# Kernel optimization log

Measured on AMD Instinct MI355X. Metric: run time of the kernel, lower is better.

Reference implementation:

```python
import jax, jax.numpy as jnp
import numpy as np

B, T, IN, H, OUT = 512, 1000, 39, 64, 48


def setup_inputs() -> dict:
    key = jax.random.key(0)
    ks = jax.random.split(key, 7)
    s = 1.0 / np.sqrt(H)
    return {
        "x": jax.random.normal(ks[0], (B, T, IN), dtype=jnp.float32),
        "W_ih": jax.random.uniform(ks[1], (4 * H, IN), minval=-s, maxval=s, dtype=jnp.float32),
        "W_hh": jax.random.uniform(ks[2], (4 * H, H), minval=-s, maxval=s, dtype=jnp.float32),
        "b_ih": jax.random.uniform(ks[3], (4 * H,), minval=-s, maxval=s, dtype=jnp.float32),
        "b_hh": jax.random.uniform(ks[4], (4 * H,), minval=-s, maxval=s, dtype=jnp.float32),
        "W_out": jax.random.uniform(ks[5], (OUT, H), minval=-s, maxval=s, dtype=jnp.float32),
        "b_out": jax.random.uniform(ks[6], (OUT,), minval=-s, maxval=s, dtype=jnp.float32),
    }


def reference(x, W_ih, W_hh, b_ih, b_hh, W_out, b_out):
    # Single-layer batch-first LSTM (zero init state) + per-step Linear + sigmoid.
    b = b_ih + b_hh  # [4H]
    # Precompute input projections for all timesteps at once: [T, B, 4H]
    xg = jnp.einsum('bti,gi->tbg', x, W_ih) + b

    def step(carry, xg_t):
        h, c = carry
        gates = xg_t + h @ W_hh.T  # [B, 4H], gate order i, f, g, o
        i, f, g, o = jnp.split(gates, 4, axis=-1)
        c = jax.nn.sigmoid(f) * c + jax.nn.sigmoid(i) * jnp.tanh(g)
        h = jax.nn.sigmoid(o) * jnp.tanh(c)
        y = jax.nn.sigmoid(h @ W_out.T + b_out)  # [B, OUT]
        return (h, c), y

    h0 = jnp.zeros((x.shape[0], W_hh.shape[1]), dtype=x.dtype)
    (_, _), ys = jax.lax.scan(step, (h0, h0), xg)  # ys: [T, B, OUT]
    return jnp.swapaxes(ys, 0, 1)  # [B, T, OUT]
```

## Files before the change

kernel.cpp:

```cpp
#include <hip/hip_runtime.h>


#define BB 512
#define TT 1000
#define INF 39
#define HH 64
#define OUTF 48
#define G4 (4 * HH)

#define Q10(M) M(0) M(1) M(2) M(3) M(4) M(5) M(6) M(7) M(8) M(9)
#define Q16(M) M(0) M(1) M(2) M(3) M(4) M(5) M(6) M(7) \
               M(8) M(9) M(10) M(11) M(12) M(13) M(14) M(15)

__global__ __launch_bounds__(256, 2) void lstm_fused_kernel(
    const float* __restrict__ x,
    const float* __restrict__ W_ih,
    const float* __restrict__ W_hh,
    const float* __restrict__ b_ih,
    const float* __restrict__ b_hh,
    const float* __restrict__ W_out,
    const float* __restrict__ b_out,
    float* __restrict__ out)
{
    const int b = blockIdx.x;
    const int tid = threadIdx.x;

    __shared__ float xs[40];
    __shared__ float hs[HH];
    __shared__ float act[G4];

    const float* wih_ptr = W_ih + tid * INF;
#define LOAD_IH4(q) float4 wiq##q; \
    wiq##q.x = wih_ptr[4*(q)]; \
    wiq##q.y = (4*(q)+1 < INF) ? wih_ptr[4*(q)+1] : 0.f; \
    wiq##q.z = (4*(q)+2 < INF) ? wih_ptr[4*(q)+2] : 0.f; \
    wiq##q.w = (4*(q)+3 < INF) ? wih_ptr[4*(q)+3] : 0.f;
    Q10(LOAD_IH4)

    const float4* wh4p = (const float4*)(W_hh + tid * HH);
#define LOAD_HH4(i) const float4 wh##i = wh4p[i];
    Q16(LOAD_HH4)

    const float bias = b_ih[tid] + b_hh[tid];

    const int o = tid >> 2;
    const int p = tid & 3;
    float4 wo0, wo1, wo2, wo3;
    float bo = 0.f;
    if (tid < 4 * OUTF) {
        const float4* wop = (const float4*)(W_out + o * HH + p * 16);
        wo0 = wop[0]; wo1 = wop[1]; wo2 = wop[2]; wo3 = wop[3];
        bo = b_out[o];
    } else {
        wo0 = wo1 = wo2 = wo3 = make_float4(0.f, 0.f, 0.f, 0.f);
    }

    float c = 0.f;
    const size_t x_base = (size_t)b * TT * INF;
    const size_t out_base = (size_t)b * TT * OUTF;

    if (tid < HH) hs[tid] = 0.f;
    if (tid < INF) xs[tid] = x[x_base + tid];
    if (tid == 39) xs[39] = 0.f;
    float xreg = (tid < INF) ? x[x_base + INF + tid] : 0.f;

    const int gate_type = tid >> 6;
    __syncthreads();

    const float4* xs4 = (const float4*)xs;
    const float4* hs4 = (const float4*)hs;

    for (int t = 0; t < TT; ++t) {
        float a0 = bias, a1 = 0.f, a2 = 0.f, a3 = 0.f;
#define FMA_IH4(q) { const float4 xv = xs4[q]; \
        a0 += xv.x * wiq##q.x; a1 += xv.y * wiq##q.y; \
        a2 += xv.z * wiq##q.z; a3 += xv.w * wiq##q.w; }
        Q10(FMA_IH4)
#define FMA_HH4(i) { const float4 hv = hs4[i]; \
        a0 += hv.x * wh##i.x; a1 += hv.y * wh##i.y; \
        a2 += hv.z * wh##i.z; a3 += hv.w * wh##i.w; }
        Q16(FMA_HH4)
        const float acc = (a0 + a1) + (a2 + a3);

        float a;
        if (gate_type == 2) {
            a = 2.f / (1.f + __expf(-2.f * acc)) - 1.f;
        } else {
            a = 1.f / (1.f + __expf(-acc));
        }
        act[tid] = a;
        __syncthreads();

        if (tid < INF) {
            xs[tid] = xreg;
            if (t + 2 < TT) xreg = x[x_base + (size_t)(t + 2) * INF + tid];
        }
        if (tid < HH) {
            const float ig = act[tid];
            const float fg = act[HH + tid];
            const float gg = act[2 * HH + tid];
            const float og = act[3 * HH + tid];
            c = fg * c + ig * gg;
            const float th = 2.f / (1.f + __expf(-2.f * c)) - 1.f;
            hs[tid] = og * th;
        }
        __syncthreads();

        if (tid < 4 * OUTF) {
            const float4 h0 = hs4[p * 4 + 0];
            const float4 h1 = hs4[p * 4 + 1];
            const float4 h2 = hs4[p * 4 + 2];
            const float4 h3 = hs4[p * 4 + 3];
            float s0 = h0.x * wo0.x + h0.y * wo0.y + h0.z * wo0.z + h0.w * wo0.w;
            float s1 = h1.x * wo1.x + h1.y * wo1.y + h1.z * wo1.z + h1.w * wo1.w;
            float s2 = h2.x * wo2.x + h2.y * wo2.y + h2.z * wo2.z + h2.w * wo2.w;
            float s3 = h3.x * wo3.x + h3.y * wo3.y + h3.z * wo3.z + h3.w * wo3.w;
            float s = (s0 + s1) + (s2 + s3);
            s += __shfl_xor(s, 1, 64);
            s += __shfl_xor(s, 2, 64);
            if (p == 0) {
                const float y = 1.f / (1.f + __expf(-(s + bo)));
                __builtin_nontemporal_store(y, &out[out_base + (size_t)t * OUTF + o]);
            }
        }
    }
}

extern "C" void kernel_launch(void* const* d_in, const int* in_sizes, int n_in,
                              void* d_out, int out_size, void* d_ws, size_t ws_size,
                              hipStream_t stream) {
    const float* x     = (const float*)d_in[0];
    const float* W_ih  = (const float*)d_in[1];
    const float* W_hh  = (const float*)d_in[2];
    const float* b_ih  = (const float*)d_in[3];
    const float* b_hh  = (const float*)d_in[4];
    const float* W_out = (const float*)d_in[5];
    const float* b_out = (const float*)d_in[6];
    float* out = (float*)d_out;

    lstm_fused_kernel<<<dim3(BB), dim3(G4), 0, stream>>>(
        x, W_ih, W_hh, b_ih, b_hh, W_out, b_out, out);
}
```

Measured before the change: 1.076 ms.

## Rewrite LSTM kernel: two sequences per block, K-split waves, one barrier per step

Each block now handles two batch rows. The 256 threads are split into 4 waves, and each wave owns a K-slice of the recurrent and input contractions for all four gates of hidden unit j. h and x values are broadcast across lanes with readlane instead of being read from shared memory. Partial sums are reduced through double-buffered shared arrays, so each timestep needs a single barrier, and the output projection is delayed by one step so it overlaps with the next step's work. A prepack kernel rearranges the weights into a gate-interleaved layout in the workspace. The trade-offs are half as many blocks, W_ih reloaded from global memory every step, and an occupancy hint of 1.

New measurement: 1.311 ms. +21.8%, slower.

```diff
diff --git a/kernel.cpp b/kernel.cpp
--- a/kernel.cpp
+++ b/kernel.cpp
@@ -6,122 +6,221 @@
 #define INF 39
 #define HH 64
 #define OUTF 48
-#define G4 (4 * HH)
-
-#define Q10(M) M(0) M(1) M(2) M(3) M(4) M(5) M(6) M(7) M(8) M(9)
-#define Q16(M) M(0) M(1) M(2) M(3) M(4) M(5) M(6) M(7) \
-               M(8) M(9) M(10) M(11) M(12) M(13) M(14) M(15)
-
-__global__ __launch_bounds__(256, 2) void lstm_fused_kernel(
-    const float* __restrict__ x,
-    const float* __restrict__ W_ih,
-    const float* __restrict__ W_hh,
-    const float* __restrict__ b_ih,
-    const float* __restrict__ b_hh,
-    const float* __restrict__ W_out,
-    const float* __restrict__ b_out,
-    float* __restrict__ out)
+
+typedef float v2f __attribute__((ext_vector_type(2)));
+
+__device__ __forceinline__ float sigf(float v)  { return 1.f / (1.f + __expf(-v)); }
+__device__ __forceinline__ float tanhx(float v) { return 2.f / (1.f + __expf(-2.f * v)) - 1.f; }
+
+#define RLF(VB, L) __int_as_float(__builtin_amdgcn_readlane((VB), (L)))
+
+__global__ void pack_weights(const float* __restrict__ W_ih,
+                             const float* __restrict__ W_hh,
+                             float4* __restrict__ ws) {
+    const int idx = blockIdx.x * 256 + threadIdx.x;
+    if (idx < 40 * 64) {
+        const int i = idx >> 6, j = idx & 63;
+        float4 v = make_float4(0.f, 0.f, 0.f, 0.f);
+        if (i < INF) {
+            v.x = W_ih[(0 * HH + j) * INF + i];
+            v.y = W_ih[(1 * HH + j) * INF + i];
+            v.z = W_ih[(2 * HH + j) * INF + i];
+            v.w = W_ih[(3 * HH + j) * INF + i];
+        }
+        ws[idx] = v;
+    } else if (idx < 40 * 64 + HH * 64) {
+        const int t = idx - 40 * 64;
+        const int k = t >> 6, j = t & 63;
+        ws[idx] = make_float4(W_hh[(0 * HH + j) * HH + k], W_hh[(1 * HH + j) * HH + k],
+                              W_hh[(2 * HH + j) * HH + k], W_hh[(3 * HH + j) * HH + k]);
+    }
+}
+
+template <bool PACKED>
+__global__ __launch_bounds__(256, 1)
+void lstm_1bar(const float* __restrict__ x,
+               const float* __restrict__ W_ih,
+               const float* __restrict__ W_hh,
+               const float* __restrict__ b_ih,
+               const float* __restrict__ b_hh,
+               const float* __restrict__ W_out,
+               const float* __restrict__ b_out,
+               const float4* __restrict__ wsq,
+               float* __restrict__ out)
 {
-    const int b = blockIdx.x;
-    const int tid = threadIdx.x;
-
-    __shared__ float xs[40];
-    __shared__ float hs[HH];
-    __shared__ float act[G4];
-
-    const float* wih_ptr = W_ih + tid * INF;
-#define LOAD_IH4(q) float4 wiq##q; \
-    wiq##q.x = wih_ptr[4*(q)]; \
-    wiq##q.y = (4*(q)+1 < INF) ? wih_ptr[4*(q)+1] : 0.f; \
-    wiq##q.z = (4*(q)+2 < INF) ? wih_ptr[4*(q)+2] : 0.f; \
-    wiq##q.w = (4*(q)+3 < INF) ? wih_ptr[4*(q)+3] : 0.f;
-    Q10(LOAD_IH4)
-
-    const float4* wh4p = (const float4*)(W_hh + tid * HH);
-#define LOAD_HH4(i) const float4 wh##i = wh4p[i];
-    Q16(LOAD_HH4)
-
-    const float bias = b_ih[tid] + b_hh[tid];
-
-    const int o = tid >> 2;
-    const int p = tid & 3;
-    float4 wo0, wo1, wo2, wo3;
+    const int tid   = threadIdx.x;
+    const int j     = tid & 63;
+    const int w     = tid >> 6;
+    const int kbase = __builtin_amdgcn_readfirstlane(16 * w);
+    const int ibase = __builtin_amdgcn_readfirstlane(10 * w);
+
+    __shared__ float4 whhG[HH * 64];
+    __shared__ float  xsb[2][2][64];
+    __shared__ float4 parts[2][4][2][64];
+    __shared__ float  yparts[2][4][2][64];
+
+    if constexpr (PACKED) {
+        const float4* src = wsq + 40 * 64;
+        for (int idx = tid; idx < HH * 64; idx += 256) whhG[idx] = src[idx];
+    } else {
+        for (int idx = tid; idx < HH * 64; idx += 256) {
+            const int k = idx >> 6, jj = idx & 63;
+            whhG[idx] = make_float4(W_hh[(0*HH+jj)*HH + k], W_hh[(1*HH+jj)*HH + k],
+                                    W_hh[(2*HH+jj)*HH + k], W_hh[(3*HH+jj)*HH + k]);
+        }
+    }
+    ((float*)xsb)[tid] = 0.f;
+
+    float woa[16];
     float bo = 0.f;
-    if (tid < 4 * OUTF) {
-        const float4* wop = (const float4*)(W_out + o * HH + p * 16);
-        wo0 = wop[0]; wo1 = wop[1]; wo2 = wop[2]; wo3 = wop[3];
-        bo = b_out[o];
+    if (j < OUTF) {
+        const float4* p = (const float4*)(W_out + j * HH + kbase);
+#pragma unroll
+        for (int q = 0; q < 4; ++q) {
+            const float4 v = p[q];
+            woa[4*q+0] = v.x; woa[4*q+1] = v.y; woa[4*q+2] = v.z; woa[4*q+3] = v.w;
+        }
+        bo = b_out[j];
     } else {
-        wo0 = wo1 = wo2 = wo3 = make_float4(0.f, 0.f, 0.f, 0.f);
-    }
-
-    float c = 0.f;
-    const size_t x_base = (size_t)b * TT * INF;
-    const size_t out_base = (size_t)b * TT * OUTF;
-
-    if (tid < HH) hs[tid] = 0.f;
-    if (tid < INF) xs[tid] = x[x_base + tid];
-    if (tid == 39) xs[39] = 0.f;
-    float xreg = (tid < INF) ? x[x_base + INF + tid] : 0.f;
-
-    const int gate_type = tid >> 6;
+#pragma unroll
+        for (int q = 0; q < 16; ++q) woa[q] = 0.f;
+    }
+
+    const float bg0 = b_ih[0*HH+j] + b_hh[0*HH+j];
+    const float bg1 = b_ih[1*HH+j] + b_hh[1*HH+j];
+    const float bg2 = b_ih[2*HH+j] + b_hh[2*HH+j];
+    const float bg3 = b_ih[3*HH+j] + b_hh[3*HH+j];
+
+    const size_t xb0 = (size_t)(2 * blockIdx.x) * TT * INF;
+    const size_t xb1 = xb0 + (size_t)TT * INF;
+    const size_t ob0 = (size_t)(2 * blockIdx.x) * TT * OUTF;
+    const size_t ob1 = ob0 + (size_t)TT * OUTF;
+
     __syncthreads();
 
-    const float4* xs4 = (const float4*)xs;
-    const float4* hs4 = (const float4*)hs;
+    float xreg = 0.f;
+    if (w == 2 && j < INF) { xsb[0][0][j] = x[xb0 + j]; xreg = x[xb0 + INF + j]; }
+    if (w == 3 && j < INF) { xsb[0][1][j] = x[xb1 + j]; xreg = x[xb1 + INF + j]; }
+
+    float h0 = 0.f, h1 = 0.f, c0 = 0.f, c1 = 0.f;
+    __syncthreads();
+
+    const float4* wkp = whhG + kbase * 64 + j;
 
     for (int t = 0; t < TT; ++t) {
-        float a0 = bias, a1 = 0.f, a2 = 0.f, a3 = 0.f;
-#define FMA_IH4(q) { const float4 xv = xs4[q]; \
-        a0 += xv.x * wiq##q.x; a1 += xv.y * wiq##q.y; \
-        a2 += xv.z * wiq##q.z; a3 += xv.w * wiq##q.w; }
-        Q10(FMA_IH4)
-#define FMA_HH4(i) { const float4 hv = hs4[i]; \
-        a0 += hv.x * wh##i.x; a1 += hv.y * wh##i.y; \
-        a2 += hv.z * wh##i.z; a3 += hv.w * wh##i.w; }
-        Q16(FMA_HH4)
-        const float acc = (a0 + a1) + (a2 + a3);
-
-        float a;
-        if (gate_type == 2) {
-            a = 2.f / (1.f + __expf(-2.f * acc)) - 1.f;
+        const int par = t & 1;
+
+        const float xr0 = xsb[par][0][j];
+        const float xr1 = xsb[par][1][j];
+        const int h0b = __float_as_int(h0), h1b = __float_as_int(h1);
+        const int x0b = __float_as_int(xr0), x1b = __float_as_int(xr1);
+
+        float4 wv[10];
+        if constexpr (PACKED) {
+#pragma unroll
+            for (int ii = 0; ii < 10; ++ii) wv[ii] = wsq[(ibase + ii) * 64 + j];
         } else {
-            a = 1.f / (1.f + __expf(-acc));
-        }
-        act[tid] = a;
+#pragma unroll
+            for (int ii = 0; ii < 10; ++ii) {
+                const int i = ibase + ii;
+                float4 v = make_float4(0.f, 0.f, 0.f, 0.f);
+                if (i < INF) {
+                    v.x = W_ih[(0*HH+j)*INF + i]; v.y = W_ih[(1*HH+j)*INF + i];
+                    v.z = W_ih[(2*HH+j)*INF + i]; v.w = W_ih[(3*HH+j)*INF + i];
+                }
+                wv[ii] = v;
+            }
+        }
+
+        if (w >= 2 && j < INF) {
+            const int r = w - 2;
+            xsb[par ^ 1][r][j] = xreg;
+            if (t + 2 < TT) xreg = x[(r ? xb1 : xb0) + (size_t)(t + 2) * INF + j];
+        }
+
+        v2f ac0_01 = {0.f,0.f}, ac0_23 = {0.f,0.f};
+        v2f ac1_01 = {0.f,0.f}, ac1_23 = {0.f,0.f};
+        v2f yac = {0.f, 0.f};
+#pragma unroll
+        for (int K = 0; K < 16; ++K) {
+            const float4 wg = wkp[K * 64];
+            const float hs0 = RLF(h0b, kbase + K);
+            const float hs1 = RLF(h1b, kbase + K);
+            ac0_01 += (v2f){wg.x, wg.y} * (v2f){hs0, hs0};
+            ac0_23 += (v2f){wg.z, wg.w} * (v2f){hs0, hs0};
+            ac1_01 += (v2f){wg.x, wg.y} * (v2f){hs1, hs1};
+            ac1_23 += (v2f){wg.z, wg.w} * (v2f){hs1, hs1};
+            yac += (v2f){hs0, hs1} * (v2f){woa[K], woa[K]};
+        }
+#pragma unroll
+        for (int ii = 0; ii < 10; ++ii) {
+            const float4 wg = wv[ii];
+            const float xs0 = RLF(x0b, ibase + ii);
+            const float xs1 = RLF(x1b, ibase + ii);
+            ac0_01 += (v2f){wg.x, wg.y} * (v2f){xs0, xs0};
+            ac0_23 += (v2f){wg.z, wg.w} * (v2f){xs0, xs0};
+            ac1_01 += (v2f){wg.x, wg.y} * (v2f){xs1, xs1};
+            ac1_23 += (v2f){wg.z, wg.w} * (v2f){xs1, xs1};
+        }
+
+        parts[par][w][0][j] = make_float4(ac0_01.x, ac0_01.y, ac0_23.x, ac0_23.y);
+        parts[par][w][1][j] = make_float4(ac1_01.x, ac1_01.y, ac1_23.x, ac1_23.y);
+        yparts[par][w][0][j] = yac.x;
+        yparts[par][w][1][j] = yac.y;
         __syncthreads();
 
-        if (tid < INF) {
-            xs[tid] = xreg;
-            if (t + 2 < TT) xreg = x[x_base + (size_t)(t + 2) * INF + tid];
-        }
-        if (tid < HH) {
-            const float ig = act[tid];
-            const float fg = act[HH + tid];
-            const float gg = act[2 * HH + tid];
-            const float og = act[3 * HH + tid];
-            c = fg * c + ig * gg;
-            const float th = 2.f / (1.f + __expf(-2.f * c)) - 1.f;
-            hs[tid] = og * th;
-        }
+        {
+            const float4 q0 = parts[par][0][0][j];
+            const float4 q1 = parts[par][1][0][j];
+            const float4 q2 = parts[par][2][0][j];
+            const float4 q3 = parts[par][3][0][j];
+            const float gi = q0.x + q1.x + q2.x + q3.x + bg0;
+            const float gf = q0.y + q1.y + q2.y + q3.y + bg1;
+            const float gg = q0.z + q1.z + q2.z + q3.z + bg2;
+            const float go = q0.w + q1.w + q2.w + q3.w + bg3;
+            c0 = fmaf(sigf(gf), c0, sigf(gi) * tanhx(gg));
+            h0 = sigf(go) * tanhx(c0);
+        }
+        {
+            const float4 q0 = parts[par][0][1][j];
+            const float4 q1 = parts[par][1][1][j];
+            const float4 q2 = parts[par][2][1][j];
+            const float4 q3 = parts[par][3][1][j];
+            const float gi = q0.x + q1.x + q2.x + q3.x + bg0;
+            const float gf = q0.y + q1.y + q2.y + q3.y + bg1;
+            const float gg = q0.z + q1.z + q2.z + q3.z + bg2;
+            const float go = q0.w + q1.w + q2.w + q3.w + bg3;
+            c1 = fmaf(sigf(gf), c1, sigf(gi) * tanhx(gg));
+            h1 = sigf(go) * tanhx(c1);
+        }
+
+        if (t >= 1 && w >= 2 && j < OUTF) {
+            const int r = w - 2;
+            const float ys = yparts[par][0][r][j] + yparts[par][1][r][j]
+                           + yparts[par][2][r][j] + yparts[par][3][r][j] + bo;
+            __builtin_nontemporal_store(sigf(ys),
+                &out[(r ? ob1 : ob0) + (size_t)(t - 1) * OUTF + j]);
+        }
+    }
+
+    {
+        const int h0b = __float_as_int(h0), h1b = __float_as_int(h1);
+        v2f yac = {0.f, 0.f};
+#pragma unroll
+        for (int K = 0; K < 16; ++K) {
+            const float hs0 = RLF(h0b, kbase + K);
+            const float hs1 = RLF(h1b, kbase + K);
+            yac += (v2f){hs0, hs1} * (v2f){woa[K], woa[K]};
+        }
+        yparts[0][w][0][j] = yac.x;
+        yparts[0][w][1][j] = yac.y;
         __syncthreads();
-
-        if (tid < 4 * OUTF) {
-            const float4 h0 = hs4[p * 4 + 0];
-            const float4 h1 = hs4[p * 4 + 1];
-            const float4 h2 = hs4[p * 4 + 2];
-            const float4 h3 = hs4[p * 4 + 3];
-            float s0 = h0.x * wo0.x + h0.y * wo0.y + h0.z * wo0.z + h0.w * wo0.w;
-            float s1 = h1.x * wo1.x + h1.y * wo1.y + h1.z * wo1.z + h1.w * wo1.w;
-            float s2 = h2.x * wo2.x + h2.y * wo2.y + h2.z * wo2.z + h2.w * wo2.w;
-            float s3 = h3.x * wo3.x + h3.y * wo3.y + h3.z * wo3.z + h3.w * wo3.w;
-            float s = (s0 + s1) + (s2 + s3);
-            s += __shfl_xor(s, 1, 64);
-            s += __shfl_xor(s, 2, 64);
-            if (p == 0) {
-                const float y = 1.f / (1.f + __expf(-(s + bo)));
-                __builtin_nontemporal_store(y, &out[out_base + (size_t)t * OUTF + o]);
-            }
+        if (w >= 2 && j < OUTF) {
+            const int r = w - 2;
+            const float ys = yparts[0][0][r][j] + yparts[0][1][r][j]
+                           + yparts[0][2][r][j] + yparts[0][3][r][j] + bo;
+            __builtin_nontemporal_store(sigf(ys),
+                &out[(r ? ob1 : ob0) + (size_t)(TT - 1) * OUTF + j]);
         }
     }
 }
@@ -129,6 +228,7 @@
 extern "C" void kernel_launch(void* const* d_in, const int* in_sizes, int n_in,
                               void* d_out, int out_size, void* d_ws, size_t ws_size,
                               hipStream_t stream) {
+    (void)in_sizes; (void)n_in; (void)out_size;
     const float* x     = (const float*)d_in[0];
     const float* W_ih  = (const float*)d_in[1];
     const float* W_hh  = (const float*)d_in[2];
@@ -138,6 +238,15 @@
     const float* b_out = (const float*)d_in[6];
     float* out = (float*)d_out;
 
-    lstm_fused_kernel<<<dim3(BB), dim3(G4), 0, stream>>>(
-        x, W_ih, W_hh, b_ih, b_hh, W_out, b_out, out);
+    float4* wsq = (float4*)d_ws;
+    const bool packed = (wsq != nullptr) && (ws_size >= (size_t)6656 * sizeof(float4));
+
+    if (packed) {
+        pack_weights<<<dim3(26), dim3(256), 0, stream>>>(W_ih, W_hh, wsq);
+        lstm_1bar<true><<<dim3(BB / 2), dim3(256), 0, stream>>>(
+            x, W_ih, W_hh, b_ih, b_hh, W_out, b_out, wsq, out);
+    } else {
+        lstm_1bar<false><<<dim3(BB / 2), dim3(256), 0, stream>>>(
+            x, W_ih, W_hh, b_ih, b_hh, W_out, b_out, nullptr, out);
+    }
 }
```
